# Performance work log

Hardware: AMD Instinct MI355X
Metric: run time of the kernel (lower is better)

## Reference

```python
import jax, jax.numpy as jnp
import numpy as np

NUDGE = 1e-7

def _norm(x):
    # global mean + L2-norm over axes (1,2), per sample (faithful to source)
    size = x.shape[1] * x.shape[2]
    mean = jnp.sum(x, axis=(1, 2), keepdims=True) / size
    xc = x - mean
    l2 = jnp.sqrt(jnp.sum(xc * xc, axis=(1, 2), keepdims=True))
    return xc / (l2 + NUDGE)


def setup_inputs() -> dict:
    key = jax.random.key(0)
    ks = jax.random.split(key, 9)
    B, D, S, F = 8, 512, 4096, 2048
    s = 0.02
    x = jax.random.normal(ks[0], (B, D, S), dtype=jnp.float32)
    Wq = jax.random.normal(ks[1], (D, D), dtype=jnp.float32) * s
    Wk = jax.random.normal(ks[2], (D, D), dtype=jnp.float32) * s
    Wv = jax.random.normal(ks[3], (D, D), dtype=jnp.float32) * s
    Wo = jax.random.normal(ks[4], (D, D), dtype=jnp.float32) * s
    W1 = jax.random.normal(ks[5], (D, F), dtype=jnp.float32) * s
    b1 = jnp.zeros((F,), dtype=jnp.float32)
    W2 = jax.random.normal(ks[6], (F, D), dtype=jnp.float32) * s
    b2 = jnp.zeros((D,), dtype=jnp.float32)
    return {"x": x, "Wq": Wq, "Wk": Wk, "Wv": Wv, "Wo": Wo,
            "W1": W1, "b1": b1, "W2": W2, "b2": b2}


def reference(x, Wq, Wk, Wv, Wo, W1, b1, W2, b2):
    B, D, S = x.shape
    xt = jnp.swapaxes(x, 1, 2)                      # [B,S,D]
    q = xt @ Wq                                     # [B,S,D]
    k = xt @ Wk
    v = xt @ Wv
    scores = jnp.einsum('bsd,btd->bst', q, k) / jnp.sqrt(jnp.float32(D))
    attn = jax.nn.softmax(scores, axis=-1)          # [B,S,S]
    attn_out = jnp.swapaxes((attn @ v) @ Wo, 1, 2)  # [B,D,S]

    post = _norm(x + attn_out)                      # [B,D,S]

    # per-slice feedforward+linear loop == batched matmul over token axis
    pt = jnp.swapaxes(post, 1, 2)                   # [B,S,D]
    h = jax.nn.relu(pt @ W1 + b1) @ W2 + b2         # [B,S,D]
    return _norm(post + jnp.swapaxes(h, 1, 2))
```

## Files before the change

kernel.cpp:

```cpp
#include <hip/hip_runtime.h>


typedef unsigned short u16;
typedef __attribute__((ext_vector_type(4))) float f32x4;
typedef __attribute__((ext_vector_type(8))) short s16x8;

__device__ __forceinline__ float bf2f(u16 u) {
    unsigned int v = ((unsigned int)u) << 16;
    float f;
    __builtin_memcpy(&f, &v, 4);
    return f;
}
__device__ __forceinline__ u16 f2bf(float f) {
    unsigned int v;
    __builtin_memcpy(&v, &f, 4);
    unsigned int r = (v + 0x7fffu + ((v >> 16) & 1u)) >> 16;
    return (u16)r;
}
__device__ __forceinline__ u16 loadbf(const void* p, long long i, int f32) {
    return f32 ? f2bf(((const float*)p)[i]) : ((const u16*)p)[i];
}

#if defined(__has_builtin)
#if __has_builtin(__builtin_amdgcn_global_load_lds)
#define HAS_GLDS 1
#endif
#endif
#ifndef HAS_GLDS
#define HAS_GLDS 0
#endif

#if HAS_GLDS
__device__ __forceinline__ void glds16(const u16* g, u16* l) {
    __builtin_amdgcn_global_load_lds(
        (const __attribute__((address_space(1))) void*)g,
        (__attribute__((address_space(3))) void*)l, 16, 0, 0);
}
#endif

__global__ __launch_bounds__(256) void detect_f32(
    const u16* __restrict__ p, int n_u16, int* __restrict__ flag)
{
    int insane = 0;
    for (int i = threadIdx.x; i < n_u16; i += 256) {
        u16 h = p[i];
        int e = (h >> 7) & 0xFF;
        int m = h & 0x7F;
        bool sane = (e >= 96 && e <= 141) || (e == 0 && m == 0);
        insane += sane ? 0 : 1;
    }
#pragma unroll
    for (int off = 32; off > 0; off >>= 1) insane += __shfl_down(insane, off);
    __shared__ int red[4];
    if ((threadIdx.x & 63) == 0) red[threadIdx.x >> 6] = insane;
    __syncthreads();
    if (threadIdx.x == 0)
        *flag = (red[0] + red[1] + red[2] + red[3] > n_u16 / 4) ? 1 : 0;
}

#define BM 128
#define BN 128
#define BK 32

template <typename OutT, bool BIAS, bool RELU>
__global__ __launch_bounds__(256) void gemm_bt(
    const u16* __restrict__ A, const u16* __restrict__ Bt, OutT* __restrict__ C,
    const u16* __restrict__ bias, int M, int N, int K,
    int lda, int ldb, int ldc, int wmod,
    long long aZ, long long aW, long long bZ, long long bW, long long cZ,
    int swz)
{
    __shared__ u16 As[2][BM * BK];
    __shared__ u16 Bs[2][BN * BK];

    const int z = blockIdx.z;
    const int g = z / wmod, w = z - g * wmod;
    A  += g * aZ + w * aW;
    Bt += g * bZ + w * bW;
    C  += (long long)z * cZ;

    int bx = blockIdx.x, by = blockIdx.y;
    if (swz) {
        int id = by * 32 + bx;
        int xcd = id & 7, i = id >> 3;
        by = xcd * 4 + (i & 3);
        bx = i >> 2;
    }

    const int tid = threadIdx.x;
    const int wave = tid >> 6, lane = tid & 63;
    const int wm = wave >> 1, wn = wave & 1;
    const int q = lane >> 4, r = lane & 15;

    const int ar = tid >> 2;
    const int ac = (tid & 3) * 8;

    const u16* Ag = A + (long long)(by * BM + ar) * lda + ac;
    const u16* Bg = Bt + (long long)(bx * BN + ar) * ldb + ac;
    const long long rstepA = 64LL * lda, rstepB = 64LL * ldb;

    f32x4 acc[4][4];
    const f32x4 zero = {0.f, 0.f, 0.f, 0.f};
#pragma unroll
    for (int i = 0; i < 4; ++i)
#pragma unroll
        for (int j = 0; j < 4; ++j) acc[i][j] = zero;

    const int nIter = K / BK;
#if HAS_GLDS
    glds16(Ag, &As[0][tid * 8]);
    glds16(Ag + rstepA, &As[0][2048 + tid * 8]);
    glds16(Bg, &Bs[0][tid * 8]);
    glds16(Bg + rstepB, &Bs[0][2048 + tid * 8]);
    Ag += BK; Bg += BK;
    __syncthreads();
    for (int it = 0; it < nIter; ++it) {
        const int cur = it & 1, nxt = cur ^ 1;
        if (it + 1 < nIter) {
            glds16(Ag, &As[nxt][tid * 8]);
            glds16(Ag + rstepA, &As[nxt][2048 + tid * 8]);
            glds16(Bg, &Bs[nxt][tid * 8]);
            glds16(Bg + rstepB, &Bs[nxt][2048 + tid * 8]);
            Ag += BK; Bg += BK;
        }
        s16x8 af[4], bf[4];
#pragma unroll
        for (int mi = 0; mi < 4; ++mi)
            af[mi] = *(const s16x8*)(&As[cur][(wm * 64 + mi * 16 + r) * BK + q * 8]);
#pragma unroll
        for (int ni = 0; ni < 4; ++ni)
            bf[ni] = *(const s16x8*)(&Bs[cur][(wn * 64 + ni * 16 + r) * BK + q * 8]);
#pragma unroll
        for (int mi = 0; mi < 4; ++mi)
#pragma unroll
            for (int ni = 0; ni < 4; ++ni)
                acc[mi][ni] = __builtin_amdgcn_mfma_f32_16x16x32_bf16(
                    af[mi], bf[ni], acc[mi][ni], 0, 0, 0);
        __syncthreads();
    }
#else
    int4 a0 = *(const int4*)(Ag);
    int4 a1 = *(const int4*)(Ag + rstepA);
    int4 b0 = *(const int4*)(Bg);
    int4 b1 = *(const int4*)(Bg + rstepB);
    for (int it = 0; it < nIter; ++it) {
        __syncthreads();
        *(int4*)(&As[0][tid * 8]) = a0;
        *(int4*)(&As[0][2048 + tid * 8]) = a1;
        *(int4*)(&Bs[0][tid * 8]) = b0;
        *(int4*)(&Bs[0][2048 + tid * 8]) = b1;
        __syncthreads();
        if (it + 1 < nIter) {
            Ag += BK; Bg += BK;
            a0 = *(const int4*)(Ag);
            a1 = *(const int4*)(Ag + rstepA);
            b0 = *(const int4*)(Bg);
            b1 = *(const int4*)(Bg + rstepB);
        }
        s16x8 af[4], bf[4];
#pragma unroll
        for (int mi = 0; mi < 4; ++mi)
            af[mi] = *(const s16x8*)(&As[0][(wm * 64 + mi * 16 + r) * BK + q * 8]);
#pragma unroll
        for (int ni = 0; ni < 4; ++ni)
            bf[ni] = *(const s16x8*)(&Bs[0][(wn * 64 + ni * 16 + r) * BK + q * 8]);
#pragma unroll
        for (int mi = 0; mi < 4; ++mi)
#pragma unroll
            for (int ni = 0; ni < 4; ++ni)
                acc[mi][ni] = __builtin_amdgcn_mfma_f32_16x16x32_bf16(
                    af[mi], bf[ni], acc[mi][ni], 0, 0, 0);
    }
#endif

    const int col0 = bx * BN + wn * 64;
    const int row0 = by * BM + wm * 64;
#pragma unroll
    for (int ni = 0; ni < 4; ++ni) {
        const int colg = col0 + ni * 16 + r;
        float bv = 0.f;
        if constexpr (BIAS) bv = bf2f(bias[colg]);
#pragma unroll
        for (int mi = 0; mi < 4; ++mi) {
#pragma unroll
            for (int rr = 0; rr < 4; ++rr) {
                const int rowg = row0 + mi * 16 + q * 4 + rr;
                float v = acc[mi][ni][rr] + bv;
                if constexpr (RELU) v = fmaxf(v, 0.f);
                if constexpr (sizeof(OutT) == 2)
                    C[(long long)rowg * ldc + colg] = (OutT)f2bf(v);
                else
                    C[(long long)rowg * ldc + colg] = (OutT)v;
            }
        }
    }
}

__global__ __launch_bounds__(256) void transpose_any(
    const void* __restrict__ in, u16* __restrict__ out, int R, int C,
    long long sIn, long long sOut, const int* __restrict__ flag)
{
    __shared__ u16 tile[32][33];
    const int f32 = *flag;
    const long long ib = (long long)blockIdx.z * sIn;
    u16* ob = out + (long long)blockIdx.z * sOut;
    const int c0 = blockIdx.x * 32, r0 = blockIdx.y * 32;
    const int tx = threadIdx.x, ty = threadIdx.y;
#pragma unroll
    for (int i = 0; i < 4; ++i) {
        int rr = ty + i * 8;
        tile[rr][tx] = loadbf(in, ib + (long long)(r0 + rr) * C + c0 + tx, f32);
    }
    __syncthreads();
#pragma unroll
    for (int i = 0; i < 4; ++i) {
        int cc = ty + i * 8;
        ob[(long long)(c0 + cc) * R + r0 + tx] = tile[tx][cc];
    }
}

__global__ __launch_bounds__(256) void transpose_b16(
    const u16* __restrict__ in, u16* __restrict__ out, int R, int C,
    long long sIn, long long sOut)
{
    __shared__ u16 tile[32][33];
    in += (long long)blockIdx.z * sIn;
    out += (long long)blockIdx.z * sOut;
    const int c0 = blockIdx.x * 32, r0 = blockIdx.y * 32;
    const int tx = threadIdx.x, ty = threadIdx.y;
#pragma unroll
    for (int i = 0; i < 4; ++i) {
        int rr = ty + i * 8;
        tile[rr][tx] = in[(long long)(r0 + rr) * C + c0 + tx];
    }
    __syncthreads();
#pragma unroll
    for (int i = 0; i < 4; ++i) {
        int cc = ty + i * 8;
        out[(long long)(c0 + cc) * R + r0 + tx] = tile[tx][cc];
    }
}

__global__ __launch_bounds__(256) void convert_bias(
    const void* __restrict__ b1, const void* __restrict__ b2,
    u16* __restrict__ ob, const int* __restrict__ f1, const int* __restrict__ f2)
{
    int i = blockIdx.x * 256 + threadIdx.x;
    if (i < 2048) ob[i] = loadbf(b1, i, *f1);
    else if (i < 2560) ob[i] = loadbf(b2, i - 2048, *f2);
}

__global__ __launch_bounds__(256) void softmax_bf16(u16* __restrict__ sc)
{
    const float scale = 0.044194173824159216f;
    u16* row = sc + (long long)blockIdx.x * 4096;
    const int tid = threadIdx.x, lane = tid & 63, wave = tid >> 6;

    u16 h[16];
    *(int4*)(h) = ((const int4*)row)[tid];
    *(int4*)(h + 8) = ((const int4*)row)[tid + 256];
    float v[16];
    float m = -3.4e38f;
#pragma unroll
    for (int j = 0; j < 16; ++j) {
        v[j] = bf2f(h[j]) * scale;
        m = fmaxf(m, v[j]);
    }
#pragma unroll
    for (int off = 32; off > 0; off >>= 1) m = fmaxf(m, __shfl_down(m, off));
    __shared__ float redm[4], reds[4];
    if (lane == 0) redm[wave] = m;
    __syncthreads();
    m = fmaxf(fmaxf(redm[0], redm[1]), fmaxf(redm[2], redm[3]));

    float s = 0.f;
#pragma unroll
    for (int j = 0; j < 16; ++j) { v[j] = __expf(v[j] - m); s += v[j]; }
#pragma unroll
    for (int off = 32; off > 0; off >>= 1) s += __shfl_down(s, off);
    if (lane == 0) reds[wave] = s;
    __syncthreads();
    s = reds[0] + reds[1] + reds[2] + reds[3];
    const float inv = 1.f / s;
#pragma unroll
    for (int j = 0; j < 16; ++j) h[j] = f2bf(v[j] * inv);
    ((int4*)row)[tid] = *(const int4*)(h);
    ((int4*)row)[tid + 256] = *(const int4*)(h + 8);
}

__global__ __launch_bounds__(256) void reduce_legs(
    const float* __restrict__ P, u16* __restrict__ O, int legs)
{
    const long long SD = 4096LL * 512;
    const int g = blockIdx.y;
    const float* Pg = P + (long long)g * legs * SD;
    u16* Og = O + (long long)g * SD;
    const int base = blockIdx.x * 2048;
#pragma unroll
    for (int it = 0; it < 8; ++it) {
        int i = base + it * 256 + threadIdx.x;
        float s = 0.f;
        for (int l = 0; l < legs; ++l) s += Pg[(long long)l * SD + i];
        Og[i] = f2bf(s);
    }
}

__global__ __launch_bounds__(256) void stats_add_partial(
    const u16* __restrict__ A, const u16* __restrict__ Bv,
    float2* __restrict__ partial)
{
    const int b = blockIdx.y;
    const long long yb = (long long)b * (4096LL * 512);
    const int base = blockIdx.x * 2048;
    float s = 0.f, ss = 0.f;
#pragma unroll
    for (int it = 0; it < 8; ++it) {
        int i = base + it * 256 + threadIdx.x;
        float z = bf2f(A[yb + i]) + bf2f(Bv[yb + i]);
        s += z; ss += z * z;
    }
#pragma unroll
    for (int off = 32; off > 0; off >>= 1) {
        s += __shfl_down(s, off); ss += __shfl_down(ss, off);
    }
    __shared__ float red[8];
    int lane = threadIdx.x & 63, wave = threadIdx.x >> 6;
    if (lane == 0) { red[wave * 2] = s; red[wave * 2 + 1] = ss; }
    __syncthreads();
    if (threadIdx.x == 0) {
        for (int w = 1; w < 4; ++w) { s += red[w * 2]; ss += red[w * 2 + 1]; }
        partial[b * 1024 + blockIdx.x] = make_float2(s, ss);
    }
}

__global__ __launch_bounds__(256) void stats_finish(
    const float2* __restrict__ partial, float2* __restrict__ stats, float N)
{
    const int b = blockIdx.x;
    float s = 0.f, ss = 0.f;
    for (int i = threadIdx.x; i < 1024; i += 256) {
        float2 p = partial[b * 1024 + i];
        s += p.x; ss += p.y;
    }
#pragma unroll
    for (int off = 32; off > 0; off >>= 1) {
        s += __shfl_down(s, off); ss += __shfl_down(ss, off);
    }
    __shared__ float red[8];
    int lane = threadIdx.x & 63, wave = threadIdx.x >> 6;
    if (lane == 0) { red[wave * 2] = s; red[wave * 2 + 1] = ss; }
    __syncthreads();
    if (threadIdx.x == 0) {
        for (int w = 1; w < 4; ++w) { s += red[w * 2]; ss += red[w * 2 + 1]; }
        float mean = s / N;
        float l2 = sqrtf(fmaxf(ss - s * s / N, 0.f));
        stats[b] = make_float2(mean, 1.f / (l2 + 1e-7f));
    }
}

__global__ __launch_bounds__(256) void post_kernel(
    const u16* __restrict__ A, const u16* __restrict__ Bv,
    const float2* __restrict__ stats, u16* __restrict__ post)
{
    const int b = blockIdx.y;
    const float2 st = stats[b];
    const long long yb = (long long)b * (4096LL * 512);
    const int base = blockIdx.x * 2048;
#pragma unroll
    for (int it = 0; it < 8; ++it) {
        int i = base + it * 256 + threadIdx.x;
        float z = bf2f(A[yb + i]) + bf2f(Bv[yb + i]);
        post[yb + i] = f2bf((z - st.x) * st.y);
    }
}

__global__ __launch_bounds__(256) void final_kernel(
    const u16* __restrict__ P, const u16* __restrict__ G,
    const float2* __restrict__ stats, float* __restrict__ out)
{
    __shared__ float tile[32][33];
    const int b = blockIdx.z;
    const float2 st = stats[b];
    const long long bb = (long long)b * (4096LL * 512);
    const int s0 = blockIdx.x * 32, d0 = blockIdx.y * 32;
    const int tx = threadIdx.x, ty = threadIdx.y;
#pragma unroll
    for (int i = 0; i < 4; ++i) {
        int sl = ty + i * 8;
        long long idx = bb + (long long)(s0 + sl) * 512 + d0 + tx;
        tile[sl][tx] = bf2f(P[idx]) + bf2f(G[idx]);
    }
    __syncthreads();
#pragma unroll
    for (int i = 0; i < 4; ++i) {
        int dl = ty + i * 8;
        out[bb + (long long)(d0 + dl) * 4096 + s0 + tx] =
            (tile[tx][dl] - st.x) * st.y;
    }
}

extern "C" void kernel_launch(void* const* d_in, const int* in_sizes, int n_in,
                              void* d_out, int out_size, void* d_ws, size_t ws_size,
                              hipStream_t stream)
{
    (void)out_size;
    const void* x  = d_in[0];
    const void* Wq = d_in[1];
    const void* Wk = d_in[2];
    const void* Wv = d_in[3];
    const void* Wo = d_in[4];
    const void* W1 = d_in[5];
    const void* b1 = d_in[6];
    const void* W2 = d_in[7];
    const void* b2 = d_in[8];

    const int Bb = 8, D = 512, S = 4096, F = 2048;
    const long long SD = (long long)S * D;
    const long long DD = (long long)D * D;
    const long long SS = (long long)S * S;

    char* ws = (char*)d_ws;
    size_t off = 0;
    auto take = [&](size_t bytes) -> char* {
        char* p = ws + off;
        off += (bytes + 255) & ~(size_t)255;
        return p;
    };
    u16* xt   = (u16*)take((size_t)Bb * SD * 2);
    u16* WqT  = (u16*)take((size_t)DD * 2);
    u16* WkT  = (u16*)take((size_t)DD * 2);
    u16* WvT  = (u16*)take((size_t)DD * 2);
    u16* WoT  = (u16*)take((size_t)DD * 2);
    u16* W1T  = (u16*)take((size_t)D * F * 2);
    u16* W2T  = (u16*)take((size_t)D * F * 2);
    u16* bb   = (u16*)take(2560 * 2);
    u16* post = (u16*)take((size_t)Bb * SD * 2);
    float2* npart  = (float2*)take(8 * 1024 * sizeof(float2));
    float2* stats1v = (float2*)take(256);
    float2* stats2v = (float2*)take(256);
    int* flags = (int*)take(16 * sizeof(int));

    size_t remaining = ws_size > off ? ws_size - off : 0;
    const size_t perG = (size_t)4 * SD * 2 + (size_t)SS * 2 + 65536;
    int G = (remaining >= 8 * perG) ? 8 : (remaining >= 4 * perG) ? 4
          : (remaining >= 2 * perG) ? 2 : 1;
    int legs = (G == 1) ? 4 : (G == 2) ? 2 : 1;

    u16* QKV    = (u16*)take((size_t)3 * G * SD * 2);
    u16* Vt     = (u16*)take((size_t)G * SD * 2);
    u16* scores = (u16*)take((size_t)G * SS * 2);
    float* partK = (float*)post;
    u16* Oall = (u16*)d_out;
    u16* Y    = scores;
    u16* Hbuf = (u16*)d_out;
    u16* Gbuf = scores;

    for (int i = 0; i < 9 && i < n_in; ++i) {
        int n = in_sizes[i] < 8192 ? in_sizes[i] : 8192;
        detect_f32<<<1, 256, 0, stream>>>((const u16*)d_in[i], n, flags + i);
    }

    dim3 tb(32, 8, 1);
    transpose_any<<<dim3(S / 32, D / 32, Bb), tb, 0, stream>>>(x, xt, D, S, SD, SD, flags + 0);
    transpose_any<<<dim3(16, 16, 1), tb, 0, stream>>>(Wq, WqT, D, D, 0, 0, flags + 1);
    transpose_any<<<dim3(16, 16, 1), tb, 0, stream>>>(Wk, WkT, D, D, 0, 0, flags + 2);
    transpose_any<<<dim3(16, 16, 1), tb, 0, stream>>>(Wv, WvT, D, D, 0, 0, flags + 3);
    transpose_any<<<dim3(16, 16, 1), tb, 0, stream>>>(Wo, WoT, D, D, 0, 0, flags + 4);
    transpose_any<<<dim3(F / 32, D / 32, 1), tb, 0, stream>>>(W1, W1T, D, F, 0, 0, flags + 5);
    transpose_any<<<dim3(D / 32, F / 32, 1), tb, 0, stream>>>(W2, W2T, F, D, 0, 0, flags + 7);
    convert_bias<<<10, 256, 0, stream>>>(b1, b2, bb, flags + 6, flags + 8);

    for (int b0 = 0; b0 < Bb; b0 += G) {
        gemm_bt<u16, false, false><<<dim3(D / 128, S / 128, 3 * G), 256, 0, stream>>>(
            xt + (long long)b0 * SD, WqT, QKV, nullptr, S, D, D, D, D, D,
            3, SD, 0, 0, DD, SD, 0);
        transpose_b16<<<dim3(D / 32, S / 32, G), tb, 0, stream>>>(
            QKV + 2 * SD, Vt, S, D, 3 * SD, SD);
        gemm_bt<u16, false, false><<<dim3(S / 128, S / 128, G), 256, 0, stream>>>(
            QKV, QKV + SD, scores, nullptr, S, S, D, D, D, S,
            1, 3 * SD, 0, 3 * SD, 0, SS, 1 );
        softmax_bf16<<<dim3(G * S), 256, 0, stream>>>(scores);
        if (legs == 1) {
            gemm_bt<u16, false, false><<<dim3(D / 128, S / 128, G), 256, 0, stream>>>(
                scores, Vt, Oall + (long long)b0 * SD, nullptr, S, D, S, S, S, D,
                1, SS, 0, SD, 0, SD, 0);
        } else {
            gemm_bt<float, false, false><<<dim3(D / 128, S / 128, G * legs), 256, 0, stream>>>(
                scores, Vt, partK, nullptr, S, D, S / legs, S, S, D,
                legs, SS, S / legs, SD, S / legs, SD, 0);
            reduce_legs<<<dim3(1024, G), 256, 0, stream>>>(
                partK, Oall + (long long)b0 * SD, legs);
        }
    }

    gemm_bt<u16, false, false><<<dim3(D / 128, (Bb * S) / 128, 1), 256, 0, stream>>>(
        Oall, WoT, Y, nullptr, Bb * S, D, D, D, D, D, 1, 0, 0, 0, 0, 0, 0);

    stats_add_partial<<<dim3(1024, Bb), 256, 0, stream>>>(xt, Y, npart);
    stats_finish<<<dim3(Bb), 256, 0, stream>>>(npart, stats1v, (float)SD);
    post_kernel<<<dim3(1024, Bb), 256, 0, stream>>>(xt, Y, stats1v, post);

    for (int h = 0; h < 2; ++h) {
        gemm_bt<u16, true, true><<<dim3(F / 128, (4 * S) / 128, 1), 256, 0, stream>>>(
            post + (long long)h * 4 * SD, W1T, Hbuf, bb, 4 * S, F, D, D, D, F,
            1, 0, 0, 0, 0, 0, 0);
        gemm_bt<u16, true, false><<<dim3(D / 128, (4 * S) / 128, 1), 256, 0, stream>>>(
            Hbuf, W2T, Gbuf + (long long)h * 4 * SD, bb + 2048, 4 * S, D, F, F, F, D,
            1, 0, 0, 0, 0, 0, 0);
    }

    stats_add_partial<<<dim3(1024, Bb), 256, 0, stream>>>(post, Gbuf, npart);
    stats_finish<<<dim3(Bb), 256, 0, stream>>>(npart, stats2v, (float)SD);
    final_kernel<<<dim3(S / 32, D / 32, Bb), tb, 0, stream>>>(
        post, Gbuf, stats2v, (float*)d_out);
}
```

Before: 1.160 ms.

## Fuse softmax exp and row-sum into QK GEMM epilogue, swizzle LDS, generalize XCD remap

Removes the standalone softmax kernel. The QK^T GEMM epilogue now writes exp(scaled score) and accumulates per-row sums with atomics, and normalisation is deferred to the PV GEMM epilogue or to reduce_legs. An XOR swizzle is added on the LDS tile columns to cut bank conflicts. The XCD-aware block remapping is generalized and enabled for all GEMMs. The exp uses no max subtraction, only a clamp at 30, so it relies on scores staying small, and the bf16 unnormalised values can lose precision.

```diff
diff --git a/kernel.cpp b/kernel.cpp
--- a/kernel.cpp
+++ b/kernel.cpp
@@ -62,13 +62,13 @@
 #define BN 128
 #define BK 32
 
-template <typename OutT, bool BIAS, bool RELU>
+template <typename OutT, bool BIAS, bool RELU, bool EXPSUM, bool RDIV>
 __global__ __launch_bounds__(256) void gemm_bt(
     const u16* __restrict__ A, const u16* __restrict__ Bt, OutT* __restrict__ C,
     const u16* __restrict__ bias, int M, int N, int K,
     int lda, int ldb, int ldc, int wmod,
     long long aZ, long long aW, long long bZ, long long bW, long long cZ,
-    int swz)
+    int swz, float* rs, long long rsZ)
 {
     __shared__ u16 As[2][BM * BK];
     __shared__ u16 Bs[2][BN * BK];
@@ -78,13 +78,15 @@
     A  += g * aZ + w * aW;
     Bt += g * bZ + w * bW;
     C  += (long long)z * cZ;
+    if (EXPSUM || RDIV) rs += z * rsZ;
 
     int bx = blockIdx.x, by = blockIdx.y;
     if (swz) {
-        int id = by * 32 + bx;
-        int xcd = id & 7, i = id >> 3;
-        by = xcd * 4 + (i & 3);
-        bx = i >> 2;
+        const int gx = gridDim.x;
+        int id = by * gx + bx;
+        int xcd = id & 7, j = id >> 3;
+        bx = j % gx;
+        by = (j / gx) * 8 + xcd;
     }
 
     const int tid = threadIdx.x;
@@ -93,7 +95,8 @@
     const int q = lane >> 4, r = lane & 15;
 
     const int ar = tid >> 2;
-    const int ac = (tid & 3) * 8;
+    const int ac = (((tid & 3) ^ ((tid >> 3) & 3)) << 3);
+    const int ks = (r >> 1) & 3;
 
     const u16* Ag = A + (long long)(by * BM + ar) * lda + ac;
     const u16* Bg = Bt + (long long)(bx * BN + ar) * ldb + ac;
@@ -126,10 +129,10 @@
         s16x8 af[4], bf[4];
 #pragma unroll
         for (int mi = 0; mi < 4; ++mi)
-            af[mi] = *(const s16x8*)(&As[cur][(wm * 64 + mi * 16 + r) * BK + q * 8]);
+            af[mi] = *(const s16x8*)(&As[cur][(wm * 64 + mi * 16 + r) * BK + ((q ^ ks) << 3)]);
 #pragma unroll
         for (int ni = 0; ni < 4; ++ni)
-            bf[ni] = *(const s16x8*)(&Bs[cur][(wn * 64 + ni * 16 + r) * BK + q * 8]);
+            bf[ni] = *(const s16x8*)(&Bs[cur][(wn * 64 + ni * 16 + r) * BK + ((q ^ ks) << 3)]);
 #pragma unroll
         for (int mi = 0; mi < 4; ++mi)
 #pragma unroll
@@ -139,31 +142,25 @@
         __syncthreads();
     }
 #else
-    int4 a0 = *(const int4*)(Ag);
-    int4 a1 = *(const int4*)(Ag + rstepA);
-    int4 b0 = *(const int4*)(Bg);
-    int4 b1 = *(const int4*)(Bg + rstepB);
     for (int it = 0; it < nIter; ++it) {
+        int4 a0 = *(const int4*)(Ag);
+        int4 a1 = *(const int4*)(Ag + rstepA);
+        int4 b0 = *(const int4*)(Bg);
+        int4 b1 = *(const int4*)(Bg + rstepB);
+        Ag += BK; Bg += BK;
         __syncthreads();
         *(int4*)(&As[0][tid * 8]) = a0;
         *(int4*)(&As[0][2048 + tid * 8]) = a1;
         *(int4*)(&Bs[0][tid * 8]) = b0;
         *(int4*)(&Bs[0][2048 + tid * 8]) = b1;
         __syncthreads();
-        if (it + 1 < nIter) {
-            Ag += BK; Bg += BK;
-            a0 = *(const int4*)(Ag);
-            a1 = *(const int4*)(Ag + rstepA);
-            b0 = *(const int4*)(Bg);
-            b1 = *(const int4*)(Bg + rstepB);
-        }
         s16x8 af[4], bf[4];
 #pragma unroll
         for (int mi = 0; mi < 4; ++mi)
-            af[mi] = *(const s16x8*)(&As[0][(wm * 64 + mi * 16 + r) * BK + q * 8]);
+            af[mi] = *(const s16x8*)(&As[0][(wm * 64 + mi * 16 + r) * BK + ((q ^ ks) << 3)]);
 #pragma unroll
         for (int ni = 0; ni < 4; ++ni)
-            bf[ni] = *(const s16x8*)(&Bs[0][(wn * 64 + ni * 16 + r) * BK + q * 8]);
+            bf[ni] = *(const s16x8*)(&Bs[0][(wn * 64 + ni * 16 + r) * BK + ((q ^ ks) << 3)]);
 #pragma unroll
         for (int mi = 0; mi < 4; ++mi)
 #pragma unroll
@@ -175,22 +172,44 @@
 
     const int col0 = bx * BN + wn * 64;
     const int row0 = by * BM + wm * 64;
-#pragma unroll
-    for (int ni = 0; ni < 4; ++ni) {
-        const int colg = col0 + ni * 16 + r;
-        float bv = 0.f;
-        if constexpr (BIAS) bv = bf2f(bias[colg]);
+    if constexpr (EXPSUM) {
+        const float scale = 0.044194173824159216f;
 #pragma unroll
         for (int mi = 0; mi < 4; ++mi) {
 #pragma unroll
             for (int rr = 0; rr < 4; ++rr) {
                 const int rowg = row0 + mi * 16 + q * 4 + rr;
-                float v = acc[mi][ni][rr] + bv;
-                if constexpr (RELU) v = fmaxf(v, 0.f);
-                if constexpr (sizeof(OutT) == 2)
-                    C[(long long)rowg * ldc + colg] = (OutT)f2bf(v);
-                else
-                    C[(long long)rowg * ldc + colg] = (OutT)v;
+                float rsum = 0.f;
+#pragma unroll
+                for (int ni = 0; ni < 4; ++ni) {
+                    float v = __expf(fminf(acc[mi][ni][rr] * scale, 30.f));
+                    rsum += v;
+                    C[(long long)rowg * ldc + col0 + ni * 16 + r] = (OutT)f2bf(v);
+                }
+#pragma unroll
+                for (int o = 1; o < 16; o <<= 1) rsum += __shfl_xor(rsum, o);
+                if (r == 0) atomicAdd(&rs[rowg], rsum);
+            }
+        }
+    } else {
+#pragma unroll
+        for (int ni = 0; ni < 4; ++ni) {
+            const int colg = col0 + ni * 16 + r;
+            float bv = 0.f;
+            if constexpr (BIAS) bv = bf2f(bias[colg]);
+#pragma unroll
+            for (int mi = 0; mi < 4; ++mi) {
+#pragma unroll
+                for (int rr = 0; rr < 4; ++rr) {
+                    const int rowg = row0 + mi * 16 + q * 4 + rr;
+                    float v = acc[mi][ni][rr] + bv;
+                    if constexpr (RELU) v = fmaxf(v, 0.f);
+                    if constexpr (RDIV) v /= rs[rowg];
+                    if constexpr (sizeof(OutT) == 2)
+                        C[(long long)rowg * ldc + colg] = (OutT)f2bf(v);
+                    else
+                        C[(long long)rowg * ldc + colg] = (OutT)v;
+                }
             }
         }
     }
@@ -250,58 +269,22 @@
     else if (i < 2560) ob[i] = loadbf(b2, i - 2048, *f2);
 }
 
-__global__ __launch_bounds__(256) void softmax_bf16(u16* __restrict__ sc)
-{
-    const float scale = 0.044194173824159216f;
-    u16* row = sc + (long long)blockIdx.x * 4096;
-    const int tid = threadIdx.x, lane = tid & 63, wave = tid >> 6;
-
-    u16 h[16];
-    *(int4*)(h) = ((const int4*)row)[tid];
-    *(int4*)(h + 8) = ((const int4*)row)[tid + 256];
-    float v[16];
-    float m = -3.4e38f;
-#pragma unroll
-    for (int j = 0; j < 16; ++j) {
-        v[j] = bf2f(h[j]) * scale;
-        m = fmaxf(m, v[j]);
-    }
-#pragma unroll
-    for (int off = 32; off > 0; off >>= 1) m = fmaxf(m, __shfl_down(m, off));
-    __shared__ float redm[4], reds[4];
-    if (lane == 0) redm[wave] = m;
-    __syncthreads();
-    m = fmaxf(fmaxf(redm[0], redm[1]), fmaxf(redm[2], redm[3]));
-
-    float s = 0.f;
-#pragma unroll
-    for (int j = 0; j < 16; ++j) { v[j] = __expf(v[j] - m); s += v[j]; }
-#pragma unroll
-    for (int off = 32; off > 0; off >>= 1) s += __shfl_down(s, off);
-    if (lane == 0) reds[wave] = s;
-    __syncthreads();
-    s = reds[0] + reds[1] + reds[2] + reds[3];
-    const float inv = 1.f / s;
-#pragma unroll
-    for (int j = 0; j < 16; ++j) h[j] = f2bf(v[j] * inv);
-    ((int4*)row)[tid] = *(const int4*)(h);
-    ((int4*)row)[tid + 256] = *(const int4*)(h + 8);
-}
-
 __global__ __launch_bounds__(256) void reduce_legs(
-    const float* __restrict__ P, u16* __restrict__ O, int legs)
+    const float* __restrict__ P, u16* __restrict__ O, int legs,
+    const float* __restrict__ l)
 {
     const long long SD = 4096LL * 512;
     const int g = blockIdx.y;
     const float* Pg = P + (long long)g * legs * SD;
+    const float* lg = l + (long long)g * 4096;
     u16* Og = O + (long long)g * SD;
     const int base = blockIdx.x * 2048;
 #pragma unroll
     for (int it = 0; it < 8; ++it) {
         int i = base + it * 256 + threadIdx.x;
         float s = 0.f;
-        for (int l = 0; l < legs; ++l) s += Pg[(long long)l * SD + i];
-        Og[i] = f2bf(s);
+        for (int lj = 0; lj < legs; ++lj) s += Pg[(long long)lj * SD + i];
+        Og[i] = f2bf(s / lg[i >> 9]);
     }
 }
 
@@ -439,6 +422,7 @@
     float2* stats1v = (float2*)take(256);
     float2* stats2v = (float2*)take(256);
     int* flags = (int*)take(16 * sizeof(int));
+    float* rowsums = (float*)take((size_t)Bb * S * sizeof(float));
 
     size_t remaining = ws_size > off ? ws_size - off : 0;
     const size_t perG = (size_t)4 * SD * 2 + (size_t)SS * 2 + 65536;
@@ -469,44 +453,44 @@
     transpose_any<<<dim3(F / 32, D / 32, 1), tb, 0, stream>>>(W1, W1T, D, F, 0, 0, flags + 5);
     transpose_any<<<dim3(D / 32, F / 32, 1), tb, 0, stream>>>(W2, W2T, F, D, 0, 0, flags + 7);
     convert_bias<<<10, 256, 0, stream>>>(b1, b2, bb, flags + 6, flags + 8);
+    hipMemsetAsync(rowsums, 0, (size_t)Bb * S * sizeof(float), stream);
 
     for (int b0 = 0; b0 < Bb; b0 += G) {
-        gemm_bt<u16, false, false><<<dim3(D / 128, S / 128, 3 * G), 256, 0, stream>>>(
+        gemm_bt<u16, false, false, false, false><<<dim3(D / 128, S / 128, 3 * G), 256, 0, stream>>>(
             xt + (long long)b0 * SD, WqT, QKV, nullptr, S, D, D, D, D, D,
-            3, SD, 0, 0, DD, SD, 0);
+            3, SD, 0, 0, DD, SD, 1, nullptr, 0);
         transpose_b16<<<dim3(D / 32, S / 32, G), tb, 0, stream>>>(
             QKV + 2 * SD, Vt, S, D, 3 * SD, SD);
-        gemm_bt<u16, false, false><<<dim3(S / 128, S / 128, G), 256, 0, stream>>>(
+        gemm_bt<u16, false, false, true, false><<<dim3(S / 128, S / 128, G), 256, 0, stream>>>(
             QKV, QKV + SD, scores, nullptr, S, S, D, D, D, S,
-            1, 3 * SD, 0, 3 * SD, 0, SS, 1 );
-        softmax_bf16<<<dim3(G * S), 256, 0, stream>>>(scores);
+            1, 3 * SD, 0, 3 * SD, 0, SS, 1, rowsums + (long long)b0 * S, S);
         if (legs == 1) {
-            gemm_bt<u16, false, false><<<dim3(D / 128, S / 128, G), 256, 0, stream>>>(
+            gemm_bt<u16, false, false, false, true><<<dim3(D / 128, S / 128, G), 256, 0, stream>>>(
                 scores, Vt, Oall + (long long)b0 * SD, nullptr, S, D, S, S, S, D,
-                1, SS, 0, SD, 0, SD, 0);
+                1, SS, 0, SD, 0, SD, 1, rowsums + (long long)b0 * S, S);
         } else {
-            gemm_bt<float, false, false><<<dim3(D / 128, S / 128, G * legs), 256, 0, stream>>>(
+            gemm_bt<float, false, false, false, false><<<dim3(D / 128, S / 128, G * legs), 256, 0, stream>>>(
                 scores, Vt, partK, nullptr, S, D, S / legs, S, S, D,
-                legs, SS, S / legs, SD, S / legs, SD, 0);
+                legs, SS, S / legs, SD, S / legs, SD, 1, nullptr, 0);
             reduce_legs<<<dim3(1024, G), 256, 0, stream>>>(
-                partK, Oall + (long long)b0 * SD, legs);
+                partK, Oall + (long long)b0 * SD, legs, rowsums + (long long)b0 * S);
         }
     }
 
-    gemm_bt<u16, false, false><<<dim3(D / 128, (Bb * S) / 128, 1), 256, 0, stream>>>(
-        Oall, WoT, Y, nullptr, Bb * S, D, D, D, D, D, 1, 0, 0, 0, 0, 0, 0);
+    gemm_bt<u16, false, false, false, false><<<dim3(D / 128, (Bb * S) / 128, 1), 256, 0, stream>>>(
+        Oall, WoT, Y, nullptr, Bb * S, D, D, D, D, D, 1, 0, 0, 0, 0, 0, 1, nullptr, 0);
 
     stats_add_partial<<<dim3(1024, Bb), 256, 0, stream>>>(xt, Y, npart);
     stats_finish<<<dim3(Bb), 256, 0, stream>>>(npart, stats1v, (float)SD);
     post_kernel<<<dim3(1024, Bb), 256, 0, stream>>>(xt, Y, stats1v, post);
 
     for (int h = 0; h < 2; ++h) {
-        gemm_bt<u16, true, true><<<dim3(F / 128, (4 * S) / 128, 1), 256, 0, stream>>>(
+        gemm_bt<u16, true, true, false, false><<<dim3(F / 128, (4 * S) / 128, 1), 256, 0, stream>>>(
             post + (long long)h * 4 * SD, W1T, Hbuf, bb, 4 * S, F, D, D, D, F,
-            1, 0, 0, 0, 0, 0, 0);
-        gemm_bt<u16, true, false><<<dim3(D / 128, (4 * S) / 128, 1), 256, 0, stream>>>(
+            1, 0, 0, 0, 0, 0, 1, nullptr, 0);
+        gemm_bt<u16, true, false, false, false><<<dim3(D / 128, (4 * S) / 128, 1), 256, 0, stream>>>(
             Hbuf, W2T, Gbuf + (long long)h * 4 * SD, bb + 2048, 4 * S, D, F, F, F, D,
-            1, 0, 0, 0, 0, 0, 0);
+            1, 0, 0, 0, 0, 0, 1, nullptr, 0);
     }
 
     stats_add_partial<<<dim3(1024, Bb), 256, 0, stream>>>(post, Gbuf, npart);
```

New measurement: 1.148 ms. Within noise of the previous version (-1.0%).
